# Performance work log

Hardware: AMD Instinct MI355X
Metric: run time of the kernel (lower is better)

The kernel has to match this reference:

```python
import jax, jax.numpy as jnp
import numpy as np

P = 16        # patch size
WIN = 64      # attention window size
NH = 12       # num heads


def _layernorm(x, g, b, eps=1e-5):
    m = x.mean(-1, keepdims=True)
    v = ((x - m) ** 2).mean(-1, keepdims=True)
    return (x - m) * jax.lax.rsqrt(v + eps) * g + b


def _sinusoidal_pe(n, d):
    pos = jnp.arange(n, dtype=jnp.float32)[:, None]
    i = jnp.arange(d // 2, dtype=jnp.float32)[None, :]
    ang = pos / jnp.power(10000.0, (2.0 * i) / d)
    pe = jnp.zeros((n, d), jnp.float32)
    pe = pe.at[:, 0::2].set(jnp.sin(ang)).at[:, 1::2].set(jnp.cos(ang))
    return pe


def setup_inputs() -> dict:
    key = jax.random.key(0)
    ks = jax.random.split(key, 8)
    B, C, H, W, D, F = 16, 3, 512, 512, 768, 3072
    s = lambda k, shape: (jax.random.normal(k, shape, jnp.float32) * 0.02)
    return {
        "input": jax.random.normal(ks[0], (B, C, H, W), jnp.float32),
        "patch_w": s(ks[1], (D, C, P, P)),
        "patch_b": jnp.zeros((D,), jnp.float32),
        "ln_g": jnp.ones((D,), jnp.float32),
        "ln_b": jnp.zeros((D,), jnp.float32),
        "qkv_w": s(ks[2], (D, 3 * D)),
        "qkv_b": jnp.zeros((3 * D,), jnp.float32),
        "proj_w": s(ks[3], (D, D)),
        "proj_b": jnp.zeros((D,), jnp.float32),
        "ff1_w": s(ks[4], (D, F)),
        "ff1_b": jnp.zeros((F,), jnp.float32),
        "ff2_w": s(ks[5], (F, D)),
        "ff2_b": jnp.zeros((D,), jnp.float32),
    }


def reference(input, patch_w, patch_b, ln_g, ln_b, qkv_w, qkv_b,
              proj_w, proj_b, ff1_w, ff1_b, ff2_w, ff2_b):
    B, C, H, W = input.shape
    D = patch_w.shape[0]
    dh = D // NH
    # --- patch embedding (conv k=stride=P as einsum) + norm ---
    xp = input.reshape(B, C, H // P, P, W // P, P)
    x = jnp.einsum('bchpwq,dcpq->bhwd', xp, patch_w) + patch_b  # [B,32,32,D]
    x = x.reshape(B, -1, D)                                      # [B,N,D]
    x = _layernorm(x, ln_g, ln_b)
    N = x.shape[1]
    # --- static sinusoidal position embedding ---
    x = x + _sinusoidal_pe(N, D)

    def ff(y):  # shared feedforward (dropout=eval/off)
        return jax.nn.gelu(y @ ff1_w + ff1_b) @ ff2_w + ff2_b

    def sparse_attn(y):  # windowed block-sparse attention, window=64
        nW = N // WIN
        qkv = (y @ qkv_w + qkv_b).reshape(B, nW, WIN, 3, NH, dh)
        q, k, v = qkv[:, :, :, 0], qkv[:, :, :, 1], qkv[:, :, :, 2]
        scores = jnp.einsum('bwqhd,bwkhd->bwhqk', q, k) * (dh ** -0.5)
        a = jax.nn.softmax(scores, axis=-1)
        o = jnp.einsum('bwhqk,bwkhd->bwqhd', a, v).reshape(B, N, D)
        return o @ proj_w + proj_b

    identity = x
    x = ff(x)
    x = sparse_attn(x)
    x = x + identity
    identity = x
    x = ff(x)
    x = x + identity
    return x
```

## Files before the change

### kernel.cpp

```cpp
#include <hip/hip_runtime.h>

typedef unsigned int uint;
typedef short bf16x8 __attribute__((ext_vector_type(8)));
typedef float f32x4 __attribute__((ext_vector_type(4)));

__device__ __forceinline__ unsigned short f2b(float f) {
    uint u = __builtin_bit_cast(uint, f);
    u += 0x7fffu + ((u >> 16) & 1u);
    return (unsigned short)(u >> 16);
}
__device__ __forceinline__ float b2f(unsigned short h) {
    uint u = ((uint)h) << 16;
    return __builtin_bit_cast(float, u);
}

__device__ __forceinline__ float fast_gelu(float v) {
    float s  = v * v;
    float t2 = __builtin_fmaf(0.044715f * s, v, v);
    float e  = __expf(-1.5957691216f * t2);
    return v * __builtin_amdgcn_rcpf(1.0f + e);
}

__device__ __forceinline__ void gl_lds16(const unsigned short* g, unsigned short* l) {
    __builtin_amdgcn_global_load_lds(
        reinterpret_cast<const __attribute__((address_space(1))) unsigned int*>(
            reinterpret_cast<uintptr_t>(g)),
        reinterpret_cast<__attribute__((address_space(3))) unsigned int*>(
            reinterpret_cast<uintptr_t>(l)),
        16, 0, 0);
}

__global__ __launch_bounds__(256) void convert_bf16_kernel(const float* __restrict__ src,
                                                           unsigned short* __restrict__ dst, int n) {
    int idx = blockIdx.x * 256 + threadIdx.x;
    if (idx < n) dst[idx] = f2b(src[idx]);
}

__global__ __launch_bounds__(256) void transpose_to_bf16_kernel(const float* __restrict__ src,
                                                                unsigned short* __restrict__ dst,
                                                                int K, int N) {
    long long idx = (long long)blockIdx.x * 256 + threadIdx.x;
    if (idx >= (long long)K * N) return;
    int k = (int)(idx / N);
    int n = (int)(idx % N);
    dst[(long long)n * K + k] = f2b(src[idx]);
}

__global__ __launch_bounds__(256) void im2col_kernel(const float* __restrict__ in,
                                                     unsigned short* __restrict__ out) {
    long long idx = (long long)blockIdx.x * 256 + threadIdx.x;
    int k = (int)(idx % 768);
    int n = (int)(idx / 768);
    int b = n >> 10, t = n & 1023;
    int hp = t >> 5, wp = t & 31;
    int c = k >> 8, rm = k & 255;
    int p = rm >> 4, q = rm & 15;
    long long src = (((long long)(b * 3 + c) * 512) + hp * 16 + p) * 512 + wp * 16 + q;
    out[idx] = f2b(in[src]);
}

__global__ __launch_bounds__(256) void ln_pe_kernel(const float* __restrict__ xe,
                                                    const float* __restrict__ g,
                                                    const float* __restrict__ bb,
                                                    unsigned short* __restrict__ xb) {
    int row = blockIdx.x;
    int pos = row & 1023;
    const float* xr = xe + (long long)row * 768;
    float v0 = xr[threadIdx.x];
    float v1 = xr[threadIdx.x + 256];
    float v2 = xr[threadIdx.x + 512];
    float s = v0 + v1 + v2;
    float sq = v0 * v0 + v1 * v1 + v2 * v2;
    for (int o = 32; o > 0; o >>= 1) {
        s  += __shfl_down(s, o, 64);
        sq += __shfl_down(sq, o, 64);
    }
    __shared__ float ps[4], pq[4];
    int w = threadIdx.x >> 6, lane = threadIdx.x & 63;
    if (lane == 0) { ps[w] = s; pq[w] = sq; }
    __syncthreads();
    float ts = ps[0] + ps[1] + ps[2] + ps[3];
    float tq = pq[0] + pq[1] + pq[2] + pq[3];
    float mean = ts * (1.0f / 768.0f);
    float var  = tq * (1.0f / 768.0f) - mean * mean;
    float inv  = rsqrtf(var + 1e-5f);
    #pragma unroll
    for (int dd = 0; dd < 3; dd++) {
        int d = threadIdx.x + dd * 256;
        float val = (dd == 0) ? v0 : (dd == 1) ? v1 : v2;
        float y = (val - mean) * inv * g[d] + bb[d];
        float freq = __expf(-(float)(d & ~1) * (9.210340371976184f / 768.0f));
        float ang = (float)pos * freq;
        y += (d & 1) ? cosf(ang) : sinf(ang);
        xb[(long long)row * 768 + d] = f2b(y);
    }
}

__global__ __launch_bounds__(512) void gemm256_kernel(const unsigned short* __restrict__ A,
                                                      const unsigned short* __restrict__ BT,
                                                      const float* __restrict__ bias,
                                                      const unsigned short* __restrict__ residB,
                                                      float* __restrict__ outF,
                                                      unsigned short* __restrict__ outB,
                                                      int M, int N, int K, int ldb,
                                                      int epi, int accumF) {
    __shared__ __align__(16) unsigned short As[2][256 * 64];
    __shared__ __align__(16) unsigned short Bs[2][256 * 64];

    const int nX = N >> 8;
    int id = blockIdx.x;
    int xcd = id & 7;
    int sq_ = id >> 3;
    int bx = sq_ % nX;
    int by = (sq_ / nX) * 8 + xcd;
    const int m0 = by * 256, n0 = bx * 256;

    const int tid = threadIdx.x;
    const int w = tid >> 6, lane = tid & 63;
    const int wr = w >> 2, wc = w & 3;
    const int quad = lane >> 4, l15 = lane & 15;
    const int swz = l15 & 7;

    const int row0 = tid >> 3;
    const int c8   = tid & 7;
    const int gc8  = c8 ^ (row0 & 7);
    const unsigned short* Ag = A  + (long long)(m0 + row0) * K   + gc8 * 8;
    const unsigned short* Bg = BT + (long long)(n0 + row0) * ldb + gc8 * 8;
    unsigned short* Ad = &As[0][0] + row0 * 64 + c8 * 8;
    unsigned short* Bd = &Bs[0][0] + row0 * 64 + c8 * 8;
    const long long aK64 = (long long)64 * K,  aK128 = (long long)128 * K;
    const long long bL64 = (long long)64 * ldb, bL128 = (long long)128 * ldb;

#define STAGE_A(bsel, h, ks) { \
    const unsigned short* s_ = Ag + (h) * aK128 + (ks); \
    unsigned short* d_ = Ad + (bsel) * 16384 + (h) * 8192; \
    gl_lds16(s_, d_); gl_lds16(s_ + aK64, d_ + 4096); }
#define STAGE_B(bsel, h, ks) { \
    const unsigned short* s_ = Bg + (h) * bL128 + (ks); \
    unsigned short* d_ = Bd + (bsel) * 16384 + (h) * 8192; \
    gl_lds16(s_, d_); gl_lds16(s_ + bL64, d_ + 4096); }

    unsigned asB = (unsigned)(uintptr_t)(&As[0][0]);
    unsigned bsB = (unsigned)(uintptr_t)(&Bs[0][0]);
    unsigned aH0 = asB + (unsigned)((wr * 64 + l15) * 128 + ((quad ^ swz) * 16));
    unsigned aH1 = asB + (unsigned)((wr * 64 + l15) * 128 + (((4 + quad) ^ swz) * 16));
    unsigned bH0 = bsB + (unsigned)((wc * 32 + l15) * 128 + ((quad ^ swz) * 16));
    unsigned bH1 = bsB + (unsigned)((wc * 32 + l15) * 128 + (((4 + quad) ^ swz) * 16));

    bf16x8 afA[4][2], afB[4][2], bfr0[2][2], bfr1[2][2];
    f32x4 acc[2][2][4][2] = {};

#define DSR(dst, addr, IMM) \
    asm volatile("ds_read_b128 %0, %1 offset:%2" : "=&v"(dst) : "v"(addr), "i"(IMM))

#define R_A0() { DSR(afA[0][0], aH0, 0);     DSR(afA[1][0], aH0, 2048); \
                 DSR(afA[2][0], aH0, 4096);  DSR(afA[3][0], aH0, 6144); \
                 DSR(afA[0][1], aH1, 0);     DSR(afA[1][1], aH1, 2048); \
                 DSR(afA[2][1], aH1, 4096);  DSR(afA[3][1], aH1, 6144); }
#define R_A1() { DSR(afB[0][0], aH0, 16384); DSR(afB[1][0], aH0, 18432); \
                 DSR(afB[2][0], aH0, 20480); DSR(afB[3][0], aH0, 22528); \
                 DSR(afB[0][1], aH1, 16384); DSR(afB[1][1], aH1, 18432); \
                 DSR(afB[2][1], aH1, 20480); DSR(afB[3][1], aH1, 22528); }
#define R_B0() { DSR(bfr0[0][0], bH0, 0);     DSR(bfr0[1][0], bH0, 2048); \
                 DSR(bfr0[0][1], bH1, 0);     DSR(bfr0[1][1], bH1, 2048); }
#define R_B1() { DSR(bfr1[0][0], bH0, 16384); DSR(bfr1[1][0], bH0, 18432); \
                 DSR(bfr1[0][1], bH1, 16384); DSR(bfr1[1][1], bH1, 18432); }

#define MFMA16(AF, BF, qm, qn) { \
    __builtin_amdgcn_sched_barrier(0); \
    __builtin_amdgcn_s_setprio(1); \
    _Pragma("unroll") for (int mf_ = 0; mf_ < 4; mf_++) \
    _Pragma("unroll") for (int nf_ = 0; nf_ < 2; nf_++) { \
      acc[qm][qn][mf_][nf_] = __builtin_amdgcn_mfma_f32_16x16x32_bf16(AF[mf_][0], BF[nf_][0], acc[qm][qn][mf_][nf_], 0, 0, 0); \
      acc[qm][qn][mf_][nf_] = __builtin_amdgcn_mfma_f32_16x16x32_bf16(AF[mf_][1], BF[nf_][1], acc[qm][qn][mf_][nf_], 0, 0, 0); \
    } \
    __builtin_amdgcn_s_setprio(0); \
    __builtin_amdgcn_sched_barrier(0); }

#define BAR() { asm volatile("" ::: "memory"); __builtin_amdgcn_s_barrier(); asm volatile("" ::: "memory"); }
#define WAITL(n) { asm volatile("s_waitcnt lgkmcnt(" #n ")" ::: "memory"); __builtin_amdgcn_sched_barrier(0); }
#define WAITV(n) { asm volatile("s_waitcnt vmcnt(" #n ")" ::: "memory"); }

    const int NT = K >> 6;

    STAGE_B(0, 0, 0);
    STAGE_A(0, 0, 0);
    STAGE_B(0, 1, 0);
    STAGE_A(0, 1, 0);
    STAGE_A(1, 0, 64);
    STAGE_B(1, 1, 64);
    STAGE_A(1, 1, 64);
    WAITV(6);
    BAR();
    R_A0();
    R_B0();

    for (int s = 0; s < NT; s++) {
        const int b = s & 1, bn = b ^ 1;
        const int ks1 = (s + 1 < NT) ? (s + 1) * 64 : 0;
        const int ks2 = (s + 2 < NT) ? (s + 2) * 64 : 0;

        R_B1();
        STAGE_B(bn, 0, ks1);
        BAR();
        WAITL(4);
        MFMA16(afA, bfr0, 0, 0);
        BAR();
        R_A1();
        STAGE_A(b, 0, ks2);
        BAR();
        WAITL(8);
        MFMA16(afA, bfr1, 0, 1);
        BAR();
        STAGE_B(b, 1, ks2);
        BAR();
        WAITL(0);
        MFMA16(afB, bfr1, 1, 1);
        WAITV(4);
        BAR();
        aH0 ^= 32768u; aH1 ^= 32768u; bH0 ^= 32768u; bH1 ^= 32768u;
        R_A0();
        MFMA16(afB, bfr0, 1, 0);
        R_B0();
        STAGE_A(b, 1, ks2);
        BAR();
    }
    asm volatile("s_waitcnt vmcnt(0) lgkmcnt(0)" ::: "memory");
    __builtin_amdgcn_sched_barrier(0);

    const int r0 = quad * 4;
    #pragma unroll
    for (int qm = 0; qm < 2; qm++)
    #pragma unroll
    for (int qn = 0; qn < 2; qn++)
    #pragma unroll
    for (int mf = 0; mf < 4; mf++)
    #pragma unroll
    for (int nf = 0; nf < 2; nf++) {
        int gn = n0 + qn * 128 + wc * 32 + nf * 16 + l15;
        float bv = bias ? bias[gn] : 0.0f;
        #pragma unroll
        for (int r = 0; r < 4; r++) {
            int gm = m0 + qm * 128 + wr * 64 + mf * 16 + r0 + r;
            float v = acc[qm][qn][mf][nf][r] + bv;
            if (epi == 1) v = fast_gelu(v);
            long long off = (long long)gm * N + gn;
            if (accumF) v += outF[off];
            if (residB) v += b2f(residB[off]);
            if (outF) outF[off] = v;
            if (outB) outB[off] = f2b(v);
        }
    }
#undef STAGE_A
#undef STAGE_B
#undef DSR
#undef R_A0
#undef R_A1
#undef R_B0
#undef R_B1
#undef MFMA16
#undef BAR
#undef WAITL
#undef WAITV
}

typedef short short8 __attribute__((ext_vector_type(8)));
__global__ __launch_bounds__(256) void attn_kernel(const unsigned short* __restrict__ qkv,
                                                   unsigned short* __restrict__ o) {
    __shared__ float qs[64 * 68];
    __shared__ float ks[64 * 68];
    __shared__ float vs[64 * 68];
    float* pmax = ks;
    float* psum = ks + 256;
    int blk = blockIdx.x;
    int h = blk % 12;
    int bw = blk / 12;
    int wi = bw % 16, b = bw / 16;
    int rowBase = b * 1024 + wi * 64;
    int tid = threadIdx.x;

    int lr = tid >> 2, c0 = (tid & 3) * 16;
    const unsigned short* src = qkv + (long long)(rowBase + lr) * 2304 + h * 64 + c0;
    #pragma unroll
    for (int half = 0; half < 2; half++) {
        short8 qv = *(const short8*)(src + half * 8);
        short8 kv = *(const short8*)(src + 768 + half * 8);
        short8 vv = *(const short8*)(src + 1536 + half * 8);
        #pragma unroll
        for (int q4 = 0; q4 < 2; q4++) {
            f32x4 qf, kf, vf;
            #pragma unroll
            for (int e = 0; e < 4; e++) {
                qf[e] = b2f((unsigned short)qv[q4 * 4 + e]);
                kf[e] = b2f((unsigned short)kv[q4 * 4 + e]);
                vf[e] = b2f((unsigned short)vv[q4 * 4 + e]);
            }
            int cc = c0 + half * 8 + q4 * 4;
            *(f32x4*)&qs[lr * 68 + cc] = qf;
            *(f32x4*)&ks[lr * 68 + cc] = kf;
            *(f32x4*)&vs[lr * 68 + cc] = vf;
        }
    }
    __syncthreads();

    int r = tid & 63, cg = tid >> 6;
    float svals[16] = {};
    for (int kk4 = 0; kk4 < 16; kk4++) {
        f32x4 qv = *(const f32x4*)&qs[r * 68 + kk4 * 4];
        #pragma unroll
        for (int j = 0; j < 16; j++) {
            f32x4 kv = *(const f32x4*)&ks[(cg * 16 + j) * 68 + kk4 * 4];
            svals[j] += qv[0] * kv[0] + qv[1] * kv[1] + qv[2] * kv[2] + qv[3] * kv[3];
        }
    }
    float smax = -1e30f;
    #pragma unroll
    for (int j = 0; j < 16; j++) {
        svals[j] *= 0.125f;
        smax = fmaxf(smax, svals[j]);
    }
    __syncthreads();
    pmax[cg * 64 + r] = smax;
    __syncthreads();
    float m = fmaxf(fmaxf(pmax[r], pmax[64 + r]), fmaxf(pmax[128 + r], pmax[192 + r]));
    float lsum = 0.0f;
    #pragma unroll
    for (int j = 0; j < 16; j++) {
        float e = __expf(svals[j] - m);
        qs[r * 68 + cg * 16 + j] = e;
        lsum += e;
    }
    psum[cg * 64 + r] = lsum;
    __syncthreads();
    float inv = __builtin_amdgcn_rcpf(psum[r] + psum[64 + r] + psum[128 + r] + psum[192 + r]);

    float oacc[16] = {};
    for (int c4 = 0; c4 < 16; c4++) {
        f32x4 pv = *(const f32x4*)&qs[r * 68 + c4 * 4];
        #pragma unroll
        for (int j4 = 0; j4 < 4; j4++) {
            f32x4 v0 = *(const f32x4*)&vs[(c4 * 4 + 0) * 68 + cg * 16 + j4 * 4];
            f32x4 v1 = *(const f32x4*)&vs[(c4 * 4 + 1) * 68 + cg * 16 + j4 * 4];
            f32x4 v2 = *(const f32x4*)&vs[(c4 * 4 + 2) * 68 + cg * 16 + j4 * 4];
            f32x4 v3 = *(const f32x4*)&vs[(c4 * 4 + 3) * 68 + cg * 16 + j4 * 4];
            #pragma unroll
            for (int e = 0; e < 4; e++)
                oacc[j4 * 4 + e] += pv[0] * v0[e] + pv[1] * v1[e] + pv[2] * v2[e] + pv[3] * v3[e];
        }
    }
    unsigned short* dst = o + (long long)(rowBase + r) * 768 + h * 64 + cg * 16;
    #pragma unroll
    for (int half = 0; half < 2; half++) {
        short8 ov;
        #pragma unroll
        for (int e = 0; e < 8; e++) ov[e] = (short)f2b(oacc[half * 8 + e] * inv);
        *(short8*)(dst + half * 8) = ov;
    }
}

extern "C" void kernel_launch(void* const* d_in, const int* in_sizes, int n_in,
                              void* d_out, int out_size, void* d_ws, size_t ws_size,
                              hipStream_t stream) {
    const float* input   = (const float*)d_in[0];
    const float* patch_w = (const float*)d_in[1];
    const float* patch_b = (const float*)d_in[2];
    const float* ln_g    = (const float*)d_in[3];
    const float* ln_b    = (const float*)d_in[4];
    const float* qkv_w   = (const float*)d_in[5];
    const float* qkv_b   = (const float*)d_in[6];
    const float* proj_w  = (const float*)d_in[7];
    const float* proj_b  = (const float*)d_in[8];
    const float* ff1_w   = (const float*)d_in[9];
    const float* ff1_b   = (const float*)d_in[10];
    const float* ff2_w   = (const float*)d_in[11];
    const float* ff2_b   = (const float*)d_in[12];
    float* out = (float*)d_out;

    const int MN = 16384;
    const int D = 768, F = 3072, TD = 2304;
    const int NY = MN / 256;

    unsigned short* wPatch = (unsigned short*)d_ws;
    unsigned short* wQkvT  = wPatch + 589824;
    unsigned short* wProjT = wQkvT + 1769472;
    unsigned short* wFf1T  = wProjT + 589824;
    unsigned short* wFf2T  = wFf1T + 2359296;
    unsigned short* bigBuf = wFf2T + 2359296;
    unsigned short* xid    = bigBuf + 50331648;
    unsigned short* t0     = xid + 12582912;

    convert_bf16_kernel<<<(589824 + 255) / 256, 256, 0, stream>>>(patch_w, wPatch, 589824);
    transpose_to_bf16_kernel<<<(1769472 + 255) / 256, 256, 0, stream>>>(qkv_w, wQkvT, D, TD);
    transpose_to_bf16_kernel<<<(589824 + 255) / 256, 256, 0, stream>>>(proj_w, wProjT, D, D);
    transpose_to_bf16_kernel<<<(2359296 + 255) / 256, 256, 0, stream>>>(ff1_w, wFf1T, D, F);
    transpose_to_bf16_kernel<<<(2359296 + 255) / 256, 256, 0, stream>>>(ff2_w, wFf2T, F, D);

    im2col_kernel<<<(MN * 768) / 256, 256, 0, stream>>>(input, bigBuf);

    gemm256_kernel<<<(D / 256) * NY, 512, 0, stream>>>(bigBuf, wPatch, patch_b, nullptr,
                                                       out, nullptr, MN, D, 768, 768, 0, 0);
    ln_pe_kernel<<<MN, 256, 0, stream>>>(out, ln_g, ln_b, xid);

    gemm256_kernel<<<(F / 256) * NY, 512, 0, stream>>>(xid, wFf1T, ff1_b, nullptr,
                                                       nullptr, bigBuf, MN, F, 768, 768, 1, 0);
    gemm256_kernel<<<(D / 256) * NY, 512, 0, stream>>>(bigBuf, wFf2T, ff2_b, nullptr,
                                                       nullptr, t0, MN, D, F, F, 0, 0);
    gemm256_kernel<<<(TD / 256) * NY, 512, 0, stream>>>(t0, wQkvT, qkv_b, nullptr,
                                                        nullptr, bigBuf, MN, TD, 768, 768, 0, 0);
    attn_kernel<<<16 * 16 * 12, 256, 0, stream>>>(bigBuf, t0);

    gemm256_kernel<<<(D / 256) * NY, 512, 0, stream>>>(t0, wProjT, proj_b, xid,
                                                       nullptr, xid, MN, D, 768, 768, 0, 0);

    gemm256_kernel<<<(F / 256) * NY, 512, 0, stream>>>(xid, wFf1T, ff1_b, nullptr,
                                                       nullptr, bigBuf, MN, F, 768, 768, 1, 0);
    gemm256_kernel<<<(D / 256) * NY, 512, 0, stream>>>(bigBuf, wFf2T, ff2_b, xid,
                                                       out, nullptr, MN, D, F, F, 0, 0);
}
```

Measured before the change: 894.5 us.

## Fuse im2col into patch-embedding GEMM and drop MFMA setprio

Replaces the separate im2col kernel and the generic GEMM for patch embedding with a dedicated GEMM that loads fp32 image patches directly, converts them to bf16 and stores them into LDS. This removes the write and re-read of a large intermediate bf16 buffer. The new kernel is single-buffered with plain synchronisation, so it may overlap loads with compute less well than the pipelined GEMM. Separately, the s_setprio calls around the MFMA blocks in the main GEMM are removed, which changes wave scheduling priority.

```diff
diff --git a/kernel.cpp b/kernel.cpp
--- a/kernel.cpp
+++ b/kernel.cpp
@@ -3,6 +3,7 @@
 typedef unsigned int uint;
 typedef short bf16x8 __attribute__((ext_vector_type(8)));
 typedef float f32x4 __attribute__((ext_vector_type(4)));
+typedef short short8 __attribute__((ext_vector_type(8)));
 
 __device__ __forceinline__ unsigned short f2b(float f) {
     uint u = __builtin_bit_cast(uint, f);
@@ -44,19 +45,6 @@
     int k = (int)(idx / N);
     int n = (int)(idx % N);
     dst[(long long)n * K + k] = f2b(src[idx]);
-}
-
-__global__ __launch_bounds__(256) void im2col_kernel(const float* __restrict__ in,
-                                                     unsigned short* __restrict__ out) {
-    long long idx = (long long)blockIdx.x * 256 + threadIdx.x;
-    int k = (int)(idx % 768);
-    int n = (int)(idx / 768);
-    int b = n >> 10, t = n & 1023;
-    int hp = t >> 5, wp = t & 31;
-    int c = k >> 8, rm = k & 255;
-    int p = rm >> 4, q = rm & 15;
-    long long src = (((long long)(b * 3 + c) * 512) + hp * 16 + p) * 512 + wp * 16 + q;
-    out[idx] = f2b(in[src]);
 }
 
 __global__ __launch_bounds__(256) void ln_pe_kernel(const float* __restrict__ xe,
@@ -96,6 +84,122 @@
     }
 }
 
+__global__ __launch_bounds__(512) void gemm_patch_kernel(const float* __restrict__ input,
+                                                         const unsigned short* __restrict__ BT,
+                                                         const float* __restrict__ bias,
+                                                         float* __restrict__ outF) {
+    __shared__ __align__(16) unsigned short As[256 * 64];
+    __shared__ __align__(16) unsigned short Bs[256 * 64];
+    const int N = 768, K = 768, ldb = 768;
+
+    const int nX = 3;
+    int id = blockIdx.x;
+    int xcd = id & 7;
+    int sq_ = id >> 3;
+    int bx = sq_ % nX;
+    int by = (sq_ / nX) * 8 + xcd;
+    const int m0 = by * 256, n0 = bx * 256;
+
+    const int tid = threadIdx.x;
+    const int w = tid >> 6, lane = tid & 63;
+    const int wr = w >> 2, wc = w & 3;
+    const int quad = lane >> 4, l15 = lane & 15;
+    const int swz = l15 & 7;
+
+    const int row0 = tid >> 3;
+    const int c8   = tid & 7;
+    const int gc8  = c8 ^ (row0 & 7);
+    const unsigned short* Bg = BT + (long long)(n0 + row0) * ldb + gc8 * 8;
+    unsigned short* Ad = As + row0 * 64 + c8 * 8;
+    unsigned short* Bd = Bs + row0 * 64 + c8 * 8;
+
+    int nb[4], nhp[4], nwp[4];
+    #pragma unroll
+    for (int hh = 0; hh < 4; hh++) {
+        int n = m0 + row0 + hh * 64;
+        nb[hh] = n >> 10;
+        int t = n & 1023;
+        nhp[hh] = t >> 5;
+        nwp[hh] = t & 31;
+    }
+
+    f32x4 acc[2][2][4][2] = {};
+
+    for (int k0 = 0; k0 < K; k0 += 64) {
+        __syncthreads();
+        int k = k0 + gc8 * 8;
+        int c = k >> 8, rm = k & 255;
+        int p = rm >> 4, q = rm & 15;
+        #pragma unroll
+        for (int hh = 0; hh < 4; hh++) {
+            const float* s = input +
+                ((((long long)nb[hh] * 3 + c) * 512) + nhp[hh] * 16 + p) * 512 + nwp[hh] * 16 + q;
+            f32x4 f0 = *(const f32x4*)s;
+            f32x4 f1 = *(const f32x4*)(s + 4);
+            bf16x8 v;
+            #pragma unroll
+            for (int e = 0; e < 4; e++) {
+                v[e]     = (short)f2b(f0[e]);
+                v[4 + e] = (short)f2b(f1[e]);
+            }
+            *(bf16x8*)(Ad + hh * 4096) = v;
+        }
+        gl_lds16(Bg + k0, Bd);
+        gl_lds16(Bg + k0 + (long long)64 * ldb,  Bd + 4096);
+        gl_lds16(Bg + k0 + (long long)128 * ldb, Bd + 8192);
+        gl_lds16(Bg + k0 + (long long)192 * ldb, Bd + 12288);
+        __syncthreads();
+
+        #pragma unroll
+        for (int qm = 0; qm < 2; qm++) {
+            bf16x8 af[4][2];
+            #pragma unroll
+            for (int mf = 0; mf < 4; mf++)
+                #pragma unroll
+                for (int kh = 0; kh < 2; kh++)
+                    af[mf][kh] = *(const bf16x8*)(As + (qm * 128 + wr * 64 + mf * 16 + l15) * 64
+                                                  + (((kh * 4 + quad) ^ swz) * 8));
+            #pragma unroll
+            for (int qn = 0; qn < 2; qn++) {
+                bf16x8 bf[2][2];
+                #pragma unroll
+                for (int nf = 0; nf < 2; nf++)
+                    #pragma unroll
+                    for (int kh = 0; kh < 2; kh++)
+                        bf[nf][kh] = *(const bf16x8*)(Bs + (qn * 128 + wc * 32 + nf * 16 + l15) * 64
+                                                      + (((kh * 4 + quad) ^ swz) * 8));
+                #pragma unroll
+                for (int mf = 0; mf < 4; mf++)
+                    #pragma unroll
+                    for (int nf = 0; nf < 2; nf++) {
+                        acc[qm][qn][mf][nf] = __builtin_amdgcn_mfma_f32_16x16x32_bf16(
+                            af[mf][0], bf[nf][0], acc[qm][qn][mf][nf], 0, 0, 0);
+                        acc[qm][qn][mf][nf] = __builtin_amdgcn_mfma_f32_16x16x32_bf16(
+                            af[mf][1], bf[nf][1], acc[qm][qn][mf][nf], 0, 0, 0);
+                    }
+            }
+        }
+    }
+
+    const int r0 = quad * 4;
+    #pragma unroll
+    for (int qm = 0; qm < 2; qm++)
+    #pragma unroll
+    for (int qn = 0; qn < 2; qn++)
+    #pragma unroll
+    for (int mf = 0; mf < 4; mf++)
+    #pragma unroll
+    for (int nf = 0; nf < 2; nf++) {
+        int gn = n0 + qn * 128 + wc * 32 + nf * 16 + l15;
+        float bv = bias[gn];
+        #pragma unroll
+        for (int r = 0; r < 4; r++) {
+            int gm = m0 + qm * 128 + wr * 64 + mf * 16 + r0 + r;
+            outF[(long long)gm * N + gn] = acc[qm][qn][mf][nf][r] + bv;
+        }
+    }
+}
+
 __global__ __launch_bounds__(512) void gemm256_kernel(const unsigned short* __restrict__ A,
                                                       const unsigned short* __restrict__ BT,
                                                       const float* __restrict__ bias,
@@ -168,13 +272,11 @@
 
 #define MFMA16(AF, BF, qm, qn) { \
     __builtin_amdgcn_sched_barrier(0); \
-    __builtin_amdgcn_s_setprio(1); \
     _Pragma("unroll") for (int mf_ = 0; mf_ < 4; mf_++) \
     _Pragma("unroll") for (int nf_ = 0; nf_ < 2; nf_++) { \
       acc[qm][qn][mf_][nf_] = __builtin_amdgcn_mfma_f32_16x16x32_bf16(AF[mf_][0], BF[nf_][0], acc[qm][qn][mf_][nf_], 0, 0, 0); \
       acc[qm][qn][mf_][nf_] = __builtin_amdgcn_mfma_f32_16x16x32_bf16(AF[mf_][1], BF[nf_][1], acc[qm][qn][mf_][nf_], 0, 0, 0); \
     } \
-    __builtin_amdgcn_s_setprio(0); \
     __builtin_amdgcn_sched_barrier(0); }
 
 #define BAR() { asm volatile("" ::: "memory"); __builtin_amdgcn_s_barrier(); asm volatile("" ::: "memory"); }
@@ -264,7 +366,6 @@
 #undef WAITV
 }
 
-typedef short short8 __attribute__((ext_vector_type(8)));
 __global__ __launch_bounds__(256) void attn_kernel(const unsigned short* __restrict__ qkv,
                                                    unsigned short* __restrict__ o) {
     __shared__ float qs[64 * 68];
@@ -395,10 +496,7 @@
     transpose_to_bf16_kernel<<<(2359296 + 255) / 256, 256, 0, stream>>>(ff1_w, wFf1T, D, F);
     transpose_to_bf16_kernel<<<(2359296 + 255) / 256, 256, 0, stream>>>(ff2_w, wFf2T, F, D);
 
-    im2col_kernel<<<(MN * 768) / 256, 256, 0, stream>>>(input, bigBuf);
-
-    gemm256_kernel<<<(D / 256) * NY, 512, 0, stream>>>(bigBuf, wPatch, patch_b, nullptr,
-                                                       out, nullptr, MN, D, 768, 768, 0, 0);
+    gemm_patch_kernel<<<(D / 256) * NY, 512, 0, stream>>>(input, wPatch, patch_b, out);
     ln_pe_kernel<<<MN, 256, 0, stream>>>(out, ln_g, ln_b, xid);
 
     gemm256_kernel<<<(F / 256) * NY, 512, 0, stream>>>(xid, wFf1T, ff1_b, nullptr,
```

New measurement: 892.3 us. About the same (-0.3%).
